# Optimization experiments

Measured on AMD Instinct MI355X. Metric: run time of the kernel, lower is better.

The kernel has to match this reference:

```python
import jax, jax.numpy as jnp
import numpy as np

N = 50000
E = 400000
IN_CH = 256
HEADS = 4
OUT_CH = 64
HID = HEADS * OUT_CH  # 256
ALPHA = 0.2
LN_EPS = 1e-5


def setup_inputs() -> dict:
    key = jax.random.key(0)
    ks = jax.random.split(key, 8)
    h = jax.random.normal(ks[0], (N, IN_CH), dtype=jnp.float32)
    edge_row = jax.random.randint(ks[1], (E,), 0, N, dtype=jnp.int32)
    edge_col = jax.random.randint(ks[2], (E,), 0, N, dtype=jnp.int32)
    # xavier-uniform-ish params
    def xavier(k, shape, fan_in, fan_out):
        lim = np.sqrt(6.0 / (fan_in + fan_out)).astype(np.float32)
        return jax.random.uniform(k, shape, jnp.float32, -lim, lim)
    W = xavier(ks[3], (IN_CH, HID), IN_CH, HID)              # Linear no bias
    attn_fc = xavier(ks[4], (HEADS, 2 * OUT_CH), 2 * OUT_CH, 1)
    ln_gamma = jnp.ones((HID,), jnp.float32)
    ln_beta = jnp.zeros((HID,), jnp.float32)
    ffn_w = xavier(ks[5], (HID, HID), HID, HID)
    ffn_b = jnp.zeros((HID,), jnp.float32)
    return {"h": h, "edge_row": edge_row, "edge_col": edge_col,
            "W": W, "attn_fc": attn_fc, "ln_gamma": ln_gamma,
            "ln_beta": ln_beta, "ffn_w": ffn_w, "ffn_b": ffn_b}


def reference(h, edge_row, edge_col, W, attn_fc, ln_gamma, ln_beta, ffn_w, ffn_b):
    # Wh: [N, H, D]
    Wh = (h @ W).reshape(N, HEADS, OUT_CH)
    Wh_i = Wh[edge_row]   # [E, H, D]
    Wh_j = Wh[edge_col]   # [E, H, D]
    # e = leakyrelu(cat(Wh_i, Wh_j) . attn_fc) per head -> split contraction
    a_src = attn_fc[:, :OUT_CH]  # [H, D]
    a_dst = attn_fc[:, OUT_CH:]  # [H, D]
    e = jnp.einsum('ehd,hd->eh', Wh_i, a_src) + jnp.einsum('ehd,hd->eh', Wh_j, a_dst)
    e = jax.nn.leaky_relu(e, negative_slope=ALPHA)
    # global max-shift exp (matches torch.exp(e - e.max(dim=0)))
    e = jnp.exp(e - jnp.max(e, axis=0, keepdims=True))  # [E, H]
    e_sum = jax.ops.segment_sum(e, edge_row, num_segments=N)  # [N, H]
    alpha = e / (e_sum[edge_row] + 1e-15)  # [E, H]  (dropout = identity in eval)
    # scatter-add weighted messages
    h_new = jax.ops.segment_sum(Wh_j * alpha[..., None], edge_row, num_segments=N)
    h_new = h_new.reshape(N, HID) + Wh.reshape(N, HID)  # residual (shapes match)
    # LayerNorm
    mu = jnp.mean(h_new, axis=-1, keepdims=True)
    var = jnp.var(h_new, axis=-1, keepdims=True)
    h_new = (h_new - mu) * jax.lax.rsqrt(var + LN_EPS) * ln_gamma + ln_beta
    # FFN: Linear + ReLU (+ dropout identity)
    return jax.nn.relu(h_new @ ffn_w + ffn_b)
```

## Files before the change

kernel.cpp:

```cpp
#include <hip/hip_runtime.h>
#include <hip/hip_bf16.h>

#define N_NODES 50000
#define E_EDGES 400000
#define IN_CH   256
#define HEADS   4
#define OUT_CH  64
#define HID     256
#define ALPHA   0.2f
#define LN_EPS  1e-5f

using f32x16 = __attribute__((ext_vector_type(16))) float;
using bf16x8 = __attribute__((ext_vector_type(8))) short;
using u16x8  = __attribute__((ext_vector_type(8))) unsigned short;
using u16x4  = __attribute__((ext_vector_type(4))) unsigned short;

typedef __attribute__((address_space(3))) void* lds_vp;
typedef const __attribute__((address_space(1))) void* gbl_vp;

__device__ __forceinline__ unsigned short f2bf(float f) {
    __hip_bfloat16 b = __float2bfloat16(f);
    return *(unsigned short*)&b;
}
__device__ __forceinline__ float bf2f(unsigned short u) {
    __hip_bfloat16 b = *(__hip_bfloat16*)&u;
    return __bfloat162float(b);
}

__global__ __launch_bounds__(256) void prep_kernel(
    const float* __restrict__ W, const float* __restrict__ ffn_w,
    unsigned short* __restrict__ Wt, unsigned short* __restrict__ Ft)
{
    int i = blockIdx.x * 256 + threadIdx.x;
    if (i < 65536) {
        int n = i >> 8, k = i & 255;
        Wt[i] = f2bf(W[k * 256 + n]);
    } else {
        int j = i - 65536;
        int n = j >> 8, k = j & 255;
        Ft[j] = f2bf(ffn_w[k * 256 + n]);
    }
}

template<bool A_IS_F32, bool RELU_BIAS>
__global__ __launch_bounds__(512, 2) void gemm_bres(
    const void* __restrict__ Av, const unsigned short* __restrict__ Bt,
    const float* __restrict__ bias, void* __restrict__ Cv, int M)
{
    __shared__ unsigned short Bs[256 * 256];

    const int tid = threadIdx.x;
    const int lane = tid & 63, wid = tid >> 6;

    #pragma unroll
    for (int i = 0; i < 16; i++) {
        int d = i * 512 + tid;
        int n = d >> 5, cp = d & 31;
        int cs = cp ^ (n & 31);
        const unsigned short* g = Bt + (size_t)n * 256 + cs * 8;
        __builtin_amdgcn_global_load_lds((gbl_vp)g, (lds_vp)&Bs[(size_t)d * 8],
                                         16, 0, 0);
    }
    __syncthreads();

    const int strip = wid * 256 + blockIdx.x;
    const int r0 = strip * 32;
    if (r0 >= M) return;

    const int q5 = lane & 31, kg = lane >> 5;
    const int rowc = min(r0 + q5, M - 1);

    f32x16 acc[8] = {};

    const float* Af = (const float*)Av;
    const unsigned short* Ab = (const unsigned short*)Av;

    float4 ra0, ra1; u16x8 rab;
    if (A_IS_F32) {
        const float* p = Af + (size_t)rowc * 256 + kg * 8;
        ra0 = *(const float4*)p; ra1 = *(const float4*)(p + 4);
    } else {
        rab = *(const u16x8*)(Ab + (size_t)rowc * 256 + kg * 8);
    }

    #pragma unroll 2
    for (int t = 0; t < 16; t++) {
        float4 nb0, nb1; u16x8 nbb;
        if (t + 1 < 16) {
            if (A_IS_F32) {
                const float* p = Af + (size_t)rowc * 256 + (t + 1) * 16 + kg * 8;
                nb0 = *(const float4*)p; nb1 = *(const float4*)(p + 4);
            } else {
                nbb = *(const u16x8*)(Ab + (size_t)rowc * 256 + (t + 1) * 16 + kg * 8);
            }
        }
        bf16x8 af;
        if (A_IS_F32) {
            union { unsigned int u[4]; bf16x8 v; } cv;
            cv.u[0] = (unsigned)f2bf(ra0.x) | ((unsigned)f2bf(ra0.y) << 16);
            cv.u[1] = (unsigned)f2bf(ra0.z) | ((unsigned)f2bf(ra0.w) << 16);
            cv.u[2] = (unsigned)f2bf(ra1.x) | ((unsigned)f2bf(ra1.y) << 16);
            cv.u[3] = (unsigned)f2bf(ra1.z) | ((unsigned)f2bf(ra1.w) << 16);
            af = cv.v;
        } else {
            union { u16x8 u; bf16x8 v; } cv; cv.u = rab; af = cv.v;
        }
        #pragma unroll
        for (int n = 0; n < 8; n++) {
            const bf16x8 bf = *(const bf16x8*)((const char*)Bs +
                (size_t)(n * 32 + q5) * 512 + (((t * 2 + kg) ^ q5) * 16));
            acc[n] = __builtin_amdgcn_mfma_f32_32x32x16_bf16(af, bf, acc[n], 0, 0, 0);
        }
        ra0 = nb0; ra1 = nb1; rab = nbb;
    }

    #pragma unroll
    for (int n = 0; n < 8; n++) {
        int gc = n * 32 + q5;
        float bv = RELU_BIAS ? bias[gc] : 0.f;
        #pragma unroll
        for (int reg = 0; reg < 16; reg++) {
            int rl = (reg & 3) + 8 * (reg >> 2) + 4 * kg;
            int gr = r0 + rl;
            if (gr >= M) continue;
            float v = acc[n][reg];
            if (RELU_BIAS) {
                v += bv; v = v > 0.f ? v : 0.f;
                ((float*)Cv)[(size_t)gr * 256 + gc] = v;
            } else {
                ((unsigned short*)Cv)[(size_t)gr * 256 + gc] = f2bf(v);
            }
        }
    }
}

__global__ __launch_bounds__(256) void scores_kernel(
    const unsigned short* __restrict__ Wh, const float* __restrict__ attn_fc,
    float* __restrict__ s_src, float* __restrict__ s_dst)
{
    const int lane = threadIdx.x & 63, wid = threadIdx.x >> 6;
    const int n = blockIdx.x * 4 + wid;
    const int h = lane >> 4;
    const int d0 = 4 * (lane & 15);
    u16x4 w = *(const u16x4*)(Wh + (size_t)n * HID + 4 * lane);
    float ps = 0.f, pd = 0.f;
    #pragma unroll
    for (int q = 0; q < 4; q++) {
        float wf = bf2f(w[q]);
        ps += wf * attn_fc[h * 128 + d0 + q];
        pd += wf * attn_fc[h * 128 + 64 + d0 + q];
    }
    #pragma unroll
    for (int off = 8; off; off >>= 1) {
        ps += __shfl_xor(ps, off, 16);
        pd += __shfl_xor(pd, off, 16);
    }
    if ((lane & 15) == 0) {
        s_src[n * HEADS + h] = ps;
        s_dst[n * HEADS + h] = pd;
    }
}

__global__ void hist_kernel(const int* __restrict__ erow, int* __restrict__ counts) {
    int e = blockIdx.x * blockDim.x + threadIdx.x;
    if (e < E_EDGES) atomicAdd(&counts[erow[e]], 1);
}

__global__ __launch_bounds__(256) void scanA_kernel(
    const int* __restrict__ counts, int* __restrict__ bsum)
{
    const int b = blockIdx.x, tid = threadIdx.x;
    int i0 = b * 512 + tid;
    int v = 0;
    if (i0 < N_NODES) v += counts[i0];
    if (i0 + 256 < N_NODES) v += counts[i0 + 256];
    #pragma unroll
    for (int off = 32; off; off >>= 1) v += __shfl_xor(v, off, 64);
    __shared__ int ws[4];
    if ((tid & 63) == 0) ws[tid >> 6] = v;
    __syncthreads();
    if (tid == 0) bsum[b] = ws[0] + ws[1] + ws[2] + ws[3];
}

__global__ __launch_bounds__(128) void scanB_kernel(
    const int* __restrict__ bsum, int* __restrict__ bscan, int nb)
{
    const int tid = threadIdx.x;
    const int lane = tid & 63, wid = tid >> 6;
    int val = (tid < nb) ? bsum[tid] : 0;
    int x = val;
    #pragma unroll
    for (int off = 1; off < 64; off <<= 1) {
        int y = __shfl_up(x, off, 64);
        if (lane >= off) x += y;
    }
    __shared__ int w0;
    if (tid == 63) w0 = x;
    __syncthreads();
    if (wid == 1) x += w0;
    if (tid < nb) bscan[tid] = x - val;
}

__global__ __launch_bounds__(512) void scanC_kernel(
    const int* __restrict__ counts, const int* __restrict__ bscan,
    int* __restrict__ offsets, int* __restrict__ cursor)
{
    const int b = blockIdx.x, tid = threadIdx.x;
    const int lane = tid & 63, wid = tid >> 6;
    const int i = b * 512 + tid;
    int v = (i < N_NODES) ? counts[i] : 0;
    int x = v;
    #pragma unroll
    for (int off = 1; off < 64; off <<= 1) {
        int y = __shfl_up(x, off, 64);
        if (lane >= off) x += y;
    }
    __shared__ int ws[8];
    if (lane == 63) ws[wid] = x;
    __syncthreads();
    if (wid == 0 && lane < 8) {
        int s = ws[lane];
        #pragma unroll
        for (int off = 1; off < 8; off <<= 1) {
            int y = __shfl_up(s, off, 8);
            if ((lane & 7) >= off) s += y;
        }
        ws[lane] = s;
    }
    __syncthreads();
    int prefix = (wid ? ws[wid - 1] : 0) + bscan[b];
    int excl = prefix + x - v;
    if (i < N_NODES) { offsets[i] = excl; cursor[i] = excl; }
    if (i == N_NODES - 1) offsets[N_NODES] = excl + v;
}

__global__ __launch_bounds__(256) void scatter_kernel(
    const int* __restrict__ erow, const int* __restrict__ ecol,
    const float* __restrict__ s_src, const float* __restrict__ s_dst,
    int* __restrict__ cursor, int* __restrict__ sorted_col,
    float4* __restrict__ sorted_w)
{
    int e = blockIdx.x * blockDim.x + threadIdx.x;
    if (e >= E_EDGES) return;
    int r = erow[e], c = ecol[e];
    float4 ss = ((const float4*)s_src)[r];
    float4 sd = ((const float4*)s_dst)[c];
    float sc[4] = {ss.x + sd.x, ss.y + sd.y, ss.z + sd.z, ss.w + sd.w};
    float4 w;
    float* wp = (float*)&w;
    #pragma unroll
    for (int h = 0; h < 4; h++) {
        float v = sc[h] > 0.f ? sc[h] : ALPHA * sc[h];
        wp[h] = __expf(v);
    }
    int pos = atomicAdd(&cursor[r], 1);
    sorted_col[pos] = c;
    sorted_w[pos] = w;
}

__global__ __launch_bounds__(256) void aggregate_ln_kernel(
    const unsigned short* __restrict__ Wh, const float* __restrict__ sorted_w,
    const int* __restrict__ offsets, const int* __restrict__ sorted_col,
    const float* __restrict__ ln_gamma, const float* __restrict__ ln_beta,
    unsigned short* __restrict__ h_ln)
{
    const int lane = threadIdx.x & 63, wid = threadIdx.x >> 6;
    const int n = blockIdx.x * 4 + wid;
    const int p = lane >> 5;
    const int q5 = lane & 31;
    const int c0 = q5 * 8;
    const int h = q5 >> 3;
    const int beg = offsets[n], end = offsets[n + 1];

    float acc[8] = {};
    float wsum = 0.f;
    for (int base = beg; base < end; base += 64) {
        int cnt = min(64, end - base);
        int cv = (base + lane < end) ? sorted_col[base + lane] : 0;
        int jj = 0;
        #pragma unroll 2
        for (; jj + 2 <= cnt; jj += 2) {
            int c = __shfl(cv, jj + p, 64);
            float w = sorted_w[(size_t)(base + jj + p) * 4 + h];
            u16x8 r = *(const u16x8*)(Wh + (size_t)c * HID + c0);
            wsum += w;
            #pragma unroll
            for (int k = 0; k < 8; k++) acc[k] += w * bf2f(r[k]);
        }
        if (jj < cnt) {
            int c = __shfl(cv, jj, 64);
            if (p == 0) {
                float w = sorted_w[(size_t)(base + jj) * 4 + h];
                u16x8 r = *(const u16x8*)(Wh + (size_t)c * HID + c0);
                wsum += w;
                #pragma unroll
                for (int k = 0; k < 8; k++) acc[k] += w * bf2f(r[k]);
            }
        }
    }
    wsum += __shfl_xor(wsum, 32, 64);
    #pragma unroll
    for (int k = 0; k < 8; k++) acc[k] += __shfl_xor(acc[k], 32, 64);

    u16x8 rr = *(const u16x8*)(Wh + (size_t)n * HID + c0);
    float inv_w = 1.f / (wsum + 1e-15f);
    float val[8];
    float s = 0.f;
    #pragma unroll
    for (int k = 0; k < 8; k++) {
        val[k] = acc[k] * inv_w + bf2f(rr[k]);
        s += val[k];
    }
    #pragma unroll
    for (int off = 16; off; off >>= 1) s += __shfl_xor(s, off, 64);
    float mu = s * (1.f / HID);
    float s2 = 0.f;
    #pragma unroll
    for (int k = 0; k < 8; k++) { float d = val[k] - mu; s2 += d * d; }
    #pragma unroll
    for (int off = 16; off; off >>= 1) s2 += __shfl_xor(s2, off, 64);
    float inv_std = rsqrtf(s2 * (1.f / HID) + LN_EPS);

    if (p == 0) {
        float4 g0 = *(const float4*)(ln_gamma + c0);
        float4 g1 = *(const float4*)(ln_gamma + c0 + 4);
        float4 b0 = *(const float4*)(ln_beta + c0);
        float4 b1 = *(const float4*)(ln_beta + c0 + 4);
        u16x8 outv;
        outv[0] = f2bf((val[0] - mu) * inv_std * g0.x + b0.x);
        outv[1] = f2bf((val[1] - mu) * inv_std * g0.y + b0.y);
        outv[2] = f2bf((val[2] - mu) * inv_std * g0.z + b0.z);
        outv[3] = f2bf((val[3] - mu) * inv_std * g0.w + b0.w);
        outv[4] = f2bf((val[4] - mu) * inv_std * g1.x + b1.x);
        outv[5] = f2bf((val[5] - mu) * inv_std * g1.y + b1.y);
        outv[6] = f2bf((val[6] - mu) * inv_std * g1.z + b1.z);
        outv[7] = f2bf((val[7] - mu) * inv_std * g1.w + b1.w);
        *(u16x8*)(h_ln + (size_t)n * HID + c0) = outv;
    }
}

extern "C" void kernel_launch(void* const* d_in, const int* in_sizes, int n_in,
                              void* d_out, int out_size, void* d_ws, size_t ws_size,
                              hipStream_t stream)
{
    const float* h        = (const float*)d_in[0];
    const int*   erow     = (const int*)  d_in[1];
    const int*   ecol     = (const int*)  d_in[2];
    const float* W        = (const float*)d_in[3];
    const float* attn_fc  = (const float*)d_in[4];
    const float* ln_gamma = (const float*)d_in[5];
    const float* ln_beta  = (const float*)d_in[6];
    const float* ffn_w    = (const float*)d_in[7];
    const float* ffn_b    = (const float*)d_in[8];
    float* out = (float*)d_out;

    unsigned short* Wh   = (unsigned short*)d_ws;
    unsigned short* h_ln = Wh + (size_t)N_NODES * HID;
    unsigned short* Wt   = h_ln + (size_t)N_NODES * HID;
    unsigned short* Ft   = Wt + 65536;
    float* s_src  = (float*)(Ft + 65536);
    float* s_dst  = s_src + N_NODES * HEADS;
    float* sorted_w = s_dst + N_NODES * HEADS;
    int*   counts = (int*)(sorted_w + (size_t)E_EDGES * HEADS);
    int*   offsets = counts + N_NODES;
    int*   cursor  = offsets + N_NODES + 1;
    int*   sorted_col = cursor + N_NODES;
    int*   bsum   = sorted_col + E_EDGES;
    int*   bscan  = bsum + 128;

    const int NB = (N_NODES + 511) / 512;

    hipMemsetAsync(counts, 0, N_NODES * sizeof(int), stream);
    prep_kernel<<<512, 256, 0, stream>>>(W, ffn_w, Wt, Ft);

    gemm_bres<true, false><<<256, 512, 0, stream>>>(h, Wt, nullptr, Wh, N_NODES);

    scores_kernel<<<N_NODES / 4, 256, 0, stream>>>(Wh, attn_fc, s_src, s_dst);
    hist_kernel<<<(E_EDGES + 255) / 256, 256, 0, stream>>>(erow, counts);
    scanA_kernel<<<NB, 256, 0, stream>>>(counts, bsum);
    scanB_kernel<<<1, 128, 0, stream>>>(bsum, bscan, NB);
    scanC_kernel<<<NB, 512, 0, stream>>>(counts, bscan, offsets, cursor);
    scatter_kernel<<<(E_EDGES + 255) / 256, 256, 0, stream>>>(
        erow, ecol, s_src, s_dst, cursor, sorted_col, (float4*)sorted_w);
    aggregate_ln_kernel<<<N_NODES / 4, 256, 0, stream>>>(
        Wh, sorted_w, offsets, sorted_col, ln_gamma, ln_beta, h_ln);

    gemm_bres<false, true><<<256, 512, 0, stream>>>(h_ln, Ft, ffn_b, out, N_NODES);
}
```

Before: 249.3 us.

## Fuse attention scores into first GEMM epilogue and deepen A-prefetch

Computes the per-node source/destination attention scores directly from the fp32 GEMM accumulators in the first GEMM's epilogue, removing the separate scores kernel and its re-read of Wh. The A-operand prefetch becomes a 4-deep register ring with the k-loop fully unrolled, to hide global load latency better. The aggregate loop unroll goes from 2 to 4. Scores are now computed from unrounded fp32 values instead of bf16 Wh, and the deeper prefetch plus score epilogue raise register pressure.

```diff
diff --git a/kernel.cpp b/kernel.cpp
--- a/kernel.cpp
+++ b/kernel.cpp
@@ -42,10 +42,12 @@
     }
 }
 
-template<bool A_IS_F32, bool RELU_BIAS>
+template<bool A_IS_F32, bool RELU_BIAS, bool SCORES>
 __global__ __launch_bounds__(512, 2) void gemm_bres(
     const void* __restrict__ Av, const unsigned short* __restrict__ Bt,
-    const float* __restrict__ bias, void* __restrict__ Cv, int M)
+    const float* __restrict__ bias, const float* __restrict__ attn_fc,
+    void* __restrict__ Cv, float* __restrict__ s_src, float* __restrict__ s_dst,
+    int M)
 {
     __shared__ unsigned short Bs[256 * 256];
 
@@ -75,43 +77,38 @@
     const float* Af = (const float*)Av;
     const unsigned short* Ab = (const unsigned short*)Av;
 
-    float4 ra0, ra1; u16x8 rab;
-    if (A_IS_F32) {
-        const float* p = Af + (size_t)rowc * 256 + kg * 8;
-        ra0 = *(const float4*)p; ra1 = *(const float4*)(p + 4);
-    } else {
-        rab = *(const u16x8*)(Ab + (size_t)rowc * 256 + kg * 8);
-    }
-
-    #pragma unroll 2
+    float4 pa[4], pb[4]; u16x8 pc[4];
+    auto loadA = [&](int t, int slot) {
+        if (A_IS_F32) {
+            const float* p = Af + (size_t)rowc * 256 + t * 16 + kg * 8;
+            pa[slot] = *(const float4*)p; pb[slot] = *(const float4*)(p + 4);
+        } else {
+            pc[slot] = *(const u16x8*)(Ab + (size_t)rowc * 256 + t * 16 + kg * 8);
+        }
+    };
+    loadA(0, 0); loadA(1, 1); loadA(2, 2); loadA(3, 3);
+
+    #pragma unroll
     for (int t = 0; t < 16; t++) {
-        float4 nb0, nb1; u16x8 nbb;
-        if (t + 1 < 16) {
-            if (A_IS_F32) {
-                const float* p = Af + (size_t)rowc * 256 + (t + 1) * 16 + kg * 8;
-                nb0 = *(const float4*)p; nb1 = *(const float4*)(p + 4);
-            } else {
-                nbb = *(const u16x8*)(Ab + (size_t)rowc * 256 + (t + 1) * 16 + kg * 8);
-            }
-        }
+        const int slot = t & 3;
         bf16x8 af;
         if (A_IS_F32) {
             union { unsigned int u[4]; bf16x8 v; } cv;
-            cv.u[0] = (unsigned)f2bf(ra0.x) | ((unsigned)f2bf(ra0.y) << 16);
-            cv.u[1] = (unsigned)f2bf(ra0.z) | ((unsigned)f2bf(ra0.w) << 16);
-            cv.u[2] = (unsigned)f2bf(ra1.x) | ((unsigned)f2bf(ra1.y) << 16);
-            cv.u[3] = (unsigned)f2bf(ra1.z) | ((unsigned)f2bf(ra1.w) << 16);
+            cv.u[0] = (unsigned)f2bf(pa[slot].x) | ((unsigned)f2bf(pa[slot].y) << 16);
+            cv.u[1] = (unsigned)f2bf(pa[slot].z) | ((unsigned)f2bf(pa[slot].w) << 16);
+            cv.u[2] = (unsigned)f2bf(pb[slot].x) | ((unsigned)f2bf(pb[slot].y) << 16);
+            cv.u[3] = (unsigned)f2bf(pb[slot].z) | ((unsigned)f2bf(pb[slot].w) << 16);
             af = cv.v;
         } else {
-            union { u16x8 u; bf16x8 v; } cv; cv.u = rab; af = cv.v;
-        }
+            union { u16x8 u; bf16x8 v; } cv; cv.u = pc[slot]; af = cv.v;
+        }
+        if (t + 4 < 16) loadA(t + 4, slot);
         #pragma unroll
         for (int n = 0; n < 8; n++) {
             const bf16x8 bf = *(const bf16x8*)((const char*)Bs +
                 (size_t)(n * 32 + q5) * 512 + (((t * 2 + kg) ^ q5) * 16));
             acc[n] = __builtin_amdgcn_mfma_f32_32x32x16_bf16(af, bf, acc[n], 0, 0, 0);
         }
-        ra0 = nb0; ra1 = nb1; rab = nbb;
     }
 
     #pragma unroll
@@ -132,32 +129,37 @@
             }
         }
     }
-}
-
-__global__ __launch_bounds__(256) void scores_kernel(
-    const unsigned short* __restrict__ Wh, const float* __restrict__ attn_fc,
-    float* __restrict__ s_src, float* __restrict__ s_dst)
-{
-    const int lane = threadIdx.x & 63, wid = threadIdx.x >> 6;
-    const int n = blockIdx.x * 4 + wid;
-    const int h = lane >> 4;
-    const int d0 = 4 * (lane & 15);
-    u16x4 w = *(const u16x4*)(Wh + (size_t)n * HID + 4 * lane);
-    float ps = 0.f, pd = 0.f;
-    #pragma unroll
-    for (int q = 0; q < 4; q++) {
-        float wf = bf2f(w[q]);
-        ps += wf * attn_fc[h * 128 + d0 + q];
-        pd += wf * attn_fc[h * 128 + 64 + d0 + q];
-    }
-    #pragma unroll
-    for (int off = 8; off; off >>= 1) {
-        ps += __shfl_xor(ps, off, 16);
-        pd += __shfl_xor(pd, off, 16);
-    }
-    if ((lane & 15) == 0) {
-        s_src[n * HEADS + h] = ps;
-        s_dst[n * HEADS + h] = pd;
+
+    if (SCORES) {
+        float as_[8], ad_[8];
+        #pragma unroll
+        for (int n = 0; n < 8; n++) {
+            int head = n >> 1, d = (n & 1) * 32 + q5;
+            as_[n] = attn_fc[head * 128 + d];
+            ad_[n] = attn_fc[head * 128 + 64 + d];
+        }
+        #pragma unroll
+        for (int reg = 0; reg < 16; reg++) {
+            int gr = r0 + (reg & 3) + 8 * (reg >> 2) + 4 * kg;
+            float ps[4] = {}, pd[4] = {};
+            #pragma unroll
+            for (int n = 0; n < 8; n++) {
+                ps[n >> 1] += acc[n][reg] * as_[n];
+                pd[n >> 1] += acc[n][reg] * ad_[n];
+            }
+            #pragma unroll
+            for (int off = 16; off; off >>= 1) {
+                #pragma unroll
+                for (int hh = 0; hh < 4; hh++) {
+                    ps[hh] += __shfl_xor(ps[hh], off, 32);
+                    pd[hh] += __shfl_xor(pd[hh], off, 32);
+                }
+            }
+            if (q5 == 0 && gr < M) {
+                *(float4*)(s_src + (size_t)gr * 4) = make_float4(ps[0], ps[1], ps[2], ps[3]);
+                *(float4*)(s_dst + (size_t)gr * 4) = make_float4(pd[0], pd[1], pd[2], pd[3]);
+            }
+        }
     }
 }
 
@@ -278,7 +280,7 @@
         int cnt = min(64, end - base);
         int cv = (base + lane < end) ? sorted_col[base + lane] : 0;
         int jj = 0;
-        #pragma unroll 2
+        #pragma unroll 4
         for (; jj + 2 <= cnt; jj += 2) {
             int c = __shfl(cv, jj + p, 64);
             float w = sorted_w[(size_t)(base + jj + p) * 4 + h];
@@ -373,9 +375,9 @@
     hipMemsetAsync(counts, 0, N_NODES * sizeof(int), stream);
     prep_kernel<<<512, 256, 0, stream>>>(W, ffn_w, Wt, Ft);
 
-    gemm_bres<true, false><<<256, 512, 0, stream>>>(h, Wt, nullptr, Wh, N_NODES);
-
-    scores_kernel<<<N_NODES / 4, 256, 0, stream>>>(Wh, attn_fc, s_src, s_dst);
+    gemm_bres<true, false, true><<<256, 512, 0, stream>>>(
+        h, Wt, nullptr, attn_fc, Wh, s_src, s_dst, N_NODES);
+
     hist_kernel<<<(E_EDGES + 255) / 256, 256, 0, stream>>>(erow, counts);
     scanA_kernel<<<NB, 256, 0, stream>>>(counts, bsum);
     scanB_kernel<<<1, 128, 0, stream>>>(bsum, bscan, NB);
@@ -385,5 +387,6 @@
     aggregate_ln_kernel<<<N_NODES / 4, 256, 0, stream>>>(
         Wh, sorted_w, offsets, sorted_col, ln_gamma, ln_beta, h_ln);
 
-    gemm_bres<false, true><<<256, 512, 0, stream>>>(h_ln, Ft, ffn_b, out, N_NODES);
-}
+    gemm_bres<false, true, false><<<256, 512, 0, stream>>>(
+        h_ln, Ft, ffn_b, nullptr, out, nullptr, nullptr, N_NODES);
+}
```

Result: no change. 252.5 us (+1.3%).

## Fuse aggregation+LayerNorm with FFN GEMM and deepen A-prefetch in GEMM

Applied to the files above, without the earlier changes.

Merges the aggregation/LayerNorm kernel with the FFN GEMM, so each 512-thread block aggregates 32 nodes into LDS and then runs the 32x256 MFMA FFN tile directly. This removes the bf16 h_ln round trip through global memory and one kernel launch. In exchange, every block reloads the full 128KB FFN weight matrix into LDS, which limits occupancy to one block per CU and costs about 1563 redundant weight loads. Separately, the first GEMM's A-operand prefetch goes from 1-deep to 4-deep with a fully unrolled loop, which raises register pressure.

```diff
diff --git a/kernel.cpp b/kernel.cpp
--- a/kernel.cpp
+++ b/kernel.cpp
@@ -75,43 +75,38 @@
     const float* Af = (const float*)Av;
     const unsigned short* Ab = (const unsigned short*)Av;
 
-    float4 ra0, ra1; u16x8 rab;
-    if (A_IS_F32) {
-        const float* p = Af + (size_t)rowc * 256 + kg * 8;
-        ra0 = *(const float4*)p; ra1 = *(const float4*)(p + 4);
-    } else {
-        rab = *(const u16x8*)(Ab + (size_t)rowc * 256 + kg * 8);
-    }
-
-    #pragma unroll 2
+    float4 pa[4], pb[4]; u16x8 pc[4];
+    auto loadA = [&](int t, int slot) {
+        if (A_IS_F32) {
+            const float* p = Af + (size_t)rowc * 256 + t * 16 + kg * 8;
+            pa[slot] = *(const float4*)p; pb[slot] = *(const float4*)(p + 4);
+        } else {
+            pc[slot] = *(const u16x8*)(Ab + (size_t)rowc * 256 + t * 16 + kg * 8);
+        }
+    };
+    loadA(0, 0); loadA(1, 1); loadA(2, 2); loadA(3, 3);
+
+    #pragma unroll
     for (int t = 0; t < 16; t++) {
-        float4 nb0, nb1; u16x8 nbb;
-        if (t + 1 < 16) {
-            if (A_IS_F32) {
-                const float* p = Af + (size_t)rowc * 256 + (t + 1) * 16 + kg * 8;
-                nb0 = *(const float4*)p; nb1 = *(const float4*)(p + 4);
-            } else {
-                nbb = *(const u16x8*)(Ab + (size_t)rowc * 256 + (t + 1) * 16 + kg * 8);
-            }
-        }
+        const int slot = t & 3;
         bf16x8 af;
         if (A_IS_F32) {
             union { unsigned int u[4]; bf16x8 v; } cv;
-            cv.u[0] = (unsigned)f2bf(ra0.x) | ((unsigned)f2bf(ra0.y) << 16);
-            cv.u[1] = (unsigned)f2bf(ra0.z) | ((unsigned)f2bf(ra0.w) << 16);
-            cv.u[2] = (unsigned)f2bf(ra1.x) | ((unsigned)f2bf(ra1.y) << 16);
-            cv.u[3] = (unsigned)f2bf(ra1.z) | ((unsigned)f2bf(ra1.w) << 16);
+            cv.u[0] = (unsigned)f2bf(pa[slot].x) | ((unsigned)f2bf(pa[slot].y) << 16);
+            cv.u[1] = (unsigned)f2bf(pa[slot].z) | ((unsigned)f2bf(pa[slot].w) << 16);
+            cv.u[2] = (unsigned)f2bf(pb[slot].x) | ((unsigned)f2bf(pb[slot].y) << 16);
+            cv.u[3] = (unsigned)f2bf(pb[slot].z) | ((unsigned)f2bf(pb[slot].w) << 16);
             af = cv.v;
         } else {
-            union { u16x8 u; bf16x8 v; } cv; cv.u = rab; af = cv.v;
-        }
+            union { u16x8 u; bf16x8 v; } cv; cv.u = pc[slot]; af = cv.v;
+        }
+        if (t + 4 < 16) loadA(t + 4, slot);
         #pragma unroll
         for (int n = 0; n < 8; n++) {
             const bf16x8 bf = *(const bf16x8*)((const char*)Bs +
                 (size_t)(n * 32 + q5) * 512 + (((t * 2 + kg) ^ q5) * 16));
             acc[n] = __builtin_amdgcn_mfma_f32_32x32x16_bf16(af, bf, acc[n], 0, 0, 0);
         }
-        ra0 = nb0; ra1 = nb1; rab = nbb;
     }
 
     #pragma unroll
@@ -258,84 +253,121 @@
     sorted_w[pos] = w;
 }
 
-__global__ __launch_bounds__(256) void aggregate_ln_kernel(
+__global__ __launch_bounds__(512) void agg_ffn_kernel(
     const unsigned short* __restrict__ Wh, const float* __restrict__ sorted_w,
     const int* __restrict__ offsets, const int* __restrict__ sorted_col,
     const float* __restrict__ ln_gamma, const float* __restrict__ ln_beta,
-    unsigned short* __restrict__ h_ln)
-{
-    const int lane = threadIdx.x & 63, wid = threadIdx.x >> 6;
-    const int n = blockIdx.x * 4 + wid;
+    const unsigned short* __restrict__ Ft, const float* __restrict__ ffn_b,
+    float* __restrict__ out)
+{
+    __shared__ unsigned short FtS[256 * 256];
+    __shared__ unsigned short Hs[32 * 256];
+
+    const int tid = threadIdx.x;
+    const int lane = tid & 63, wid = tid >> 6;
+
+    #pragma unroll
+    for (int i = 0; i < 16; i++) {
+        int d = i * 512 + tid;
+        int n = d >> 5, cp = d & 31;
+        int cs = cp ^ (n & 31);
+        const unsigned short* g = Ft + (size_t)n * 256 + cs * 8;
+        __builtin_amdgcn_global_load_lds((gbl_vp)g, (lds_vp)&FtS[(size_t)d * 8],
+                                         16, 0, 0);
+    }
+
+    const int n0 = blockIdx.x * 32;
     const int p = lane >> 5;
     const int q5 = lane & 31;
     const int c0 = q5 * 8;
     const int h = q5 >> 3;
-    const int beg = offsets[n], end = offsets[n + 1];
-
-    float acc[8] = {};
-    float wsum = 0.f;
-    for (int base = beg; base < end; base += 64) {
-        int cnt = min(64, end - base);
-        int cv = (base + lane < end) ? sorted_col[base + lane] : 0;
-        int jj = 0;
-        #pragma unroll 2
-        for (; jj + 2 <= cnt; jj += 2) {
-            int c = __shfl(cv, jj + p, 64);
-            float w = sorted_w[(size_t)(base + jj + p) * 4 + h];
-            u16x8 r = *(const u16x8*)(Wh + (size_t)c * HID + c0);
-            wsum += w;
-            #pragma unroll
-            for (int k = 0; k < 8; k++) acc[k] += w * bf2f(r[k]);
-        }
-        if (jj < cnt) {
-            int c = __shfl(cv, jj, 64);
-            if (p == 0) {
-                float w = sorted_w[(size_t)(base + jj) * 4 + h];
+
+    for (int nd = 0; nd < 4; nd++) {
+        const int lrow = wid * 4 + nd;
+        const int n = n0 + lrow;
+        if (n >= N_NODES) continue;
+        const int beg = offsets[n], end = offsets[n + 1];
+
+        float acc[8] = {};
+        float wsum = 0.f;
+        for (int base = beg; base < end; base += 64) {
+            int cnt = min(64, end - base);
+            int cv = (base + lane < end) ? sorted_col[base + lane] : 0;
+            int jj = 0;
+            #pragma unroll 2
+            for (; jj + 2 <= cnt; jj += 2) {
+                int c = __shfl(cv, jj + p, 64);
+                float w = sorted_w[(size_t)(base + jj + p) * 4 + h];
                 u16x8 r = *(const u16x8*)(Wh + (size_t)c * HID + c0);
                 wsum += w;
                 #pragma unroll
                 for (int k = 0; k < 8; k++) acc[k] += w * bf2f(r[k]);
             }
-        }
-    }
-    wsum += __shfl_xor(wsum, 32, 64);
-    #pragma unroll
-    for (int k = 0; k < 8; k++) acc[k] += __shfl_xor(acc[k], 32, 64);
-
-    u16x8 rr = *(const u16x8*)(Wh + (size_t)n * HID + c0);
-    float inv_w = 1.f / (wsum + 1e-15f);
-    float val[8];
-    float s = 0.f;
-    #pragma unroll
-    for (int k = 0; k < 8; k++) {
-        val[k] = acc[k] * inv_w + bf2f(rr[k]);
-        s += val[k];
-    }
-    #pragma unroll
-    for (int off = 16; off; off >>= 1) s += __shfl_xor(s, off, 64);
-    float mu = s * (1.f / HID);
-    float s2 = 0.f;
-    #pragma unroll
-    for (int k = 0; k < 8; k++) { float d = val[k] - mu; s2 += d * d; }
-    #pragma unroll
-    for (int off = 16; off; off >>= 1) s2 += __shfl_xor(s2, off, 64);
-    float inv_std = rsqrtf(s2 * (1.f / HID) + LN_EPS);
-
-    if (p == 0) {
-        float4 g0 = *(const float4*)(ln_gamma + c0);
-        float4 g1 = *(const float4*)(ln_gamma + c0 + 4);
-        float4 b0 = *(const float4*)(ln_beta + c0);
-        float4 b1 = *(const float4*)(ln_beta + c0 + 4);
-        u16x8 outv;
-        outv[0] = f2bf((val[0] - mu) * inv_std * g0.x + b0.x);
-        outv[1] = f2bf((val[1] - mu) * inv_std * g0.y + b0.y);
-        outv[2] = f2bf((val[2] - mu) * inv_std * g0.z + b0.z);
-        outv[3] = f2bf((val[3] - mu) * inv_std * g0.w + b0.w);
-        outv[4] = f2bf((val[4] - mu) * inv_std * g1.x + b1.x);
-        outv[5] = f2bf((val[5] - mu) * inv_std * g1.y + b1.y);
-        outv[6] = f2bf((val[6] - mu) * inv_std * g1.z + b1.z);
-        outv[7] = f2bf((val[7] - mu) * inv_std * g1.w + b1.w);
-        *(u16x8*)(h_ln + (size_t)n * HID + c0) = outv;
+            if (jj < cnt) {
+                int c = __shfl(cv, jj, 64);
+                if (p == 0) {
+                    float w = sorted_w[(size_t)(base + jj) * 4 + h];
+                    u16x8 r = *(const u16x8*)(Wh + (size_t)c * HID + c0);
+                    wsum += w;
+                    #pragma unroll
+                    for (int k = 0; k < 8; k++) acc[k] += w * bf2f(r[k]);
+                }
+            }
+        }
+        wsum += __shfl_xor(wsum, 32, 64);
+        #pragma unroll
+        for (int k = 0; k < 8; k++) acc[k] += __shfl_xor(acc[k], 32, 64);
+
+        u16x8 rr = *(const u16x8*)(Wh + (size_t)n * HID + c0);
+        float inv_w = 1.f / (wsum + 1e-15f);
+        float val[8];
+        float s = 0.f;
+        #pragma unroll
+        for (int k = 0; k < 8; k++) {
+            val[k] = acc[k] * inv_w + bf2f(rr[k]);
+            s += val[k];
+        }
+        #pragma unroll
+        for (int off = 16; off; off >>= 1) s += __shfl_xor(s, off, 64);
+        float mu = s * (1.f / HID);
+        float s2 = 0.f;
+        #pragma unroll
+        for (int k = 0; k < 8; k++) { float d = val[k] - mu; s2 += d * d; }
+        #pragma unroll
+        for (int off = 16; off; off >>= 1) s2 += __shfl_xor(s2, off, 64);
+        float inv_std = rsqrtf(s2 * (1.f / HID) + LN_EPS);
+
+        if (p == 0) {
+            u16x8 o;
+            #pragma unroll
+            for (int k = 0; k < 8; k++)
+                o[k] = f2bf((val[k] - mu) * inv_std * ln_gamma[c0 + k] + ln_beta[c0 + k]);
+            *(u16x8*)((char*)Hs + lrow * 512 + ((q5 ^ lrow) * 16)) = o;
+        }
+    }
+
+    __syncthreads();
+
+    const int kg = lane >> 5;
+    f32x16 acc2 = {};
+    #pragma unroll
+    for (int t = 0; t < 16; t++) {
+        const bf16x8 afr = *(const bf16x8*)((const char*)Hs +
+            q5 * 512 + (((t * 2 + kg) ^ q5) * 16));
+        const bf16x8 bfr = *(const bf16x8*)((const char*)FtS +
+            (size_t)(wid * 32 + q5) * 512 + (((t * 2 + kg) ^ q5) * 16));
+        acc2 = __builtin_amdgcn_mfma_f32_32x32x16_bf16(afr, bfr, acc2, 0, 0, 0);
+    }
+    const int gc = wid * 32 + q5;
+    const float bv = ffn_b[gc];
+    #pragma unroll
+    for (int reg = 0; reg < 16; reg++) {
+        int rl = (reg & 3) + 8 * (reg >> 2) + 4 * kg;
+        int gr = n0 + rl;
+        if (gr >= N_NODES) continue;
+        float v = acc2[reg] + bv;
+        v = v > 0.f ? v : 0.f;
+        out[(size_t)gr * 256 + gc] = v;
     }
 }
 
@@ -355,8 +387,7 @@
     float* out = (float*)d_out;
 
     unsigned short* Wh   = (unsigned short*)d_ws;
-    unsigned short* h_ln = Wh + (size_t)N_NODES * HID;
-    unsigned short* Wt   = h_ln + (size_t)N_NODES * HID;
+    unsigned short* Wt   = Wh + (size_t)N_NODES * HID;
     unsigned short* Ft   = Wt + 65536;
     float* s_src  = (float*)(Ft + 65536);
     float* s_dst  = s_src + N_NODES * HEADS;
@@ -369,6 +400,7 @@
     int*   bscan  = bsum + 128;
 
     const int NB = (N_NODES + 511) / 512;
+    const int GRID_AGG = (N_NODES + 31) / 32;
 
     hipMemsetAsync(counts, 0, N_NODES * sizeof(int), stream);
     prep_kernel<<<512, 256, 0, stream>>>(W, ffn_w, Wt, Ft);
@@ -382,8 +414,7 @@
     scanC_kernel<<<NB, 512, 0, stream>>>(counts, bscan, offsets, cursor);
     scatter_kernel<<<(E_EDGES + 255) / 256, 256, 0, stream>>>(
         erow, ecol, s_src, s_dst, cursor, sorted_col, (float4*)sorted_w);
-    aggregate_ln_kernel<<<N_NODES / 4, 256, 0, stream>>>(
-        Wh, sorted_w, offsets, sorted_col, ln_gamma, ln_beta, h_ln);
-
-    gemm_bres<false, true><<<256, 512, 0, stream>>>(h_ln, Ft, ffn_b, out, N_NODES);
-}
+
+    agg_ffn_kernel<<<GRID_AGG, 512, 0, stream>>>(
+        Wh, sorted_w, offsets, sorted_col, ln_gamma, ln_beta, Ft, ffn_b, out);
+}
```

Result: slower. 309.6 us (+24.2%).

## Split GEMM output columns across two blocks and double-buffer A loads

Applied to the files above, without the earlier changes.

Each GEMM block now computes only half of the 256 output columns, so the B tile held in LDS shrinks to 64KB. The grid doubles to 512 blocks and the launch bound allows 4 blocks per CU, which raises occupancy and spreads work across more CUs. The A-row prefetch becomes a two-deep register buffer loaded two k-steps ahead. The cost is that each A row is read twice, once per column half, and every block still loads its own B half.

```diff
diff --git a/kernel.cpp b/kernel.cpp
--- a/kernel.cpp
+++ b/kernel.cpp
@@ -43,80 +43,78 @@
 }
 
 template<bool A_IS_F32, bool RELU_BIAS>
-__global__ __launch_bounds__(512, 2) void gemm_bres(
+__global__ __launch_bounds__(512, 4) void gemm_bres(
     const void* __restrict__ Av, const unsigned short* __restrict__ Bt,
     const float* __restrict__ bias, void* __restrict__ Cv, int M)
 {
-    __shared__ unsigned short Bs[256 * 256];
+    __shared__ unsigned short Bs[128 * 256];
 
     const int tid = threadIdx.x;
     const int lane = tid & 63, wid = tid >> 6;
-
-    #pragma unroll
-    for (int i = 0; i < 16; i++) {
+    const int colhalf = blockIdx.x & 1;
+    const int col0 = colhalf * 128;
+    const int sb = blockIdx.x >> 1;
+
+    #pragma unroll
+    for (int i = 0; i < 8; i++) {
         int d = i * 512 + tid;
         int n = d >> 5, cp = d & 31;
         int cs = cp ^ (n & 31);
-        const unsigned short* g = Bt + (size_t)n * 256 + cs * 8;
+        const unsigned short* g = Bt + (size_t)(col0 + n) * 256 + cs * 8;
         __builtin_amdgcn_global_load_lds((gbl_vp)g, (lds_vp)&Bs[(size_t)d * 8],
                                          16, 0, 0);
     }
     __syncthreads();
 
-    const int strip = wid * 256 + blockIdx.x;
+    const int strip = wid * 256 + sb;
     const int r0 = strip * 32;
     if (r0 >= M) return;
 
     const int q5 = lane & 31, kg = lane >> 5;
     const int rowc = min(r0 + q5, M - 1);
 
-    f32x16 acc[8] = {};
+    f32x16 acc[4] = {};
 
     const float* Af = (const float*)Av;
     const unsigned short* Ab = (const unsigned short*)Av;
 
-    float4 ra0, ra1; u16x8 rab;
-    if (A_IS_F32) {
-        const float* p = Af + (size_t)rowc * 256 + kg * 8;
-        ra0 = *(const float4*)p; ra1 = *(const float4*)(p + 4);
-    } else {
-        rab = *(const u16x8*)(Ab + (size_t)rowc * 256 + kg * 8);
-    }
-
-    #pragma unroll 2
+    float4 pa[2], pb[2]; u16x8 pc[2];
+    auto loadA = [&](int t, int slot) {
+        if (A_IS_F32) {
+            const float* p = Af + (size_t)rowc * 256 + t * 16 + kg * 8;
+            pa[slot] = *(const float4*)p; pb[slot] = *(const float4*)(p + 4);
+        } else {
+            pc[slot] = *(const u16x8*)(Ab + (size_t)rowc * 256 + t * 16 + kg * 8);
+        }
+    };
+    loadA(0, 0); loadA(1, 1);
+
+    #pragma unroll
     for (int t = 0; t < 16; t++) {
-        float4 nb0, nb1; u16x8 nbb;
-        if (t + 1 < 16) {
-            if (A_IS_F32) {
-                const float* p = Af + (size_t)rowc * 256 + (t + 1) * 16 + kg * 8;
-                nb0 = *(const float4*)p; nb1 = *(const float4*)(p + 4);
-            } else {
-                nbb = *(const u16x8*)(Ab + (size_t)rowc * 256 + (t + 1) * 16 + kg * 8);
-            }
-        }
+        const int slot = t & 1;
         bf16x8 af;
         if (A_IS_F32) {
             union { unsigned int u[4]; bf16x8 v; } cv;
-            cv.u[0] = (unsigned)f2bf(ra0.x) | ((unsigned)f2bf(ra0.y) << 16);
-            cv.u[1] = (unsigned)f2bf(ra0.z) | ((unsigned)f2bf(ra0.w) << 16);
-            cv.u[2] = (unsigned)f2bf(ra1.x) | ((unsigned)f2bf(ra1.y) << 16);
-            cv.u[3] = (unsigned)f2bf(ra1.z) | ((unsigned)f2bf(ra1.w) << 16);
+            cv.u[0] = (unsigned)f2bf(pa[slot].x) | ((unsigned)f2bf(pa[slot].y) << 16);
+            cv.u[1] = (unsigned)f2bf(pa[slot].z) | ((unsigned)f2bf(pa[slot].w) << 16);
+            cv.u[2] = (unsigned)f2bf(pb[slot].x) | ((unsigned)f2bf(pb[slot].y) << 16);
+            cv.u[3] = (unsigned)f2bf(pb[slot].z) | ((unsigned)f2bf(pb[slot].w) << 16);
             af = cv.v;
         } else {
-            union { u16x8 u; bf16x8 v; } cv; cv.u = rab; af = cv.v;
-        }
+            union { u16x8 u; bf16x8 v; } cv; cv.u = pc[slot]; af = cv.v;
+        }
+        if (t + 2 < 16) loadA(t + 2, slot);
         #pragma unroll
-        for (int n = 0; n < 8; n++) {
+        for (int n = 0; n < 4; n++) {
             const bf16x8 bf = *(const bf16x8*)((const char*)Bs +
                 (size_t)(n * 32 + q5) * 512 + (((t * 2 + kg) ^ q5) * 16));
             acc[n] = __builtin_amdgcn_mfma_f32_32x32x16_bf16(af, bf, acc[n], 0, 0, 0);
         }
-        ra0 = nb0; ra1 = nb1; rab = nbb;
-    }
-
-    #pragma unroll
-    for (int n = 0; n < 8; n++) {
-        int gc = n * 32 + q5;
+    }
+
+    #pragma unroll
+    for (int n = 0; n < 4; n++) {
+        int gc = col0 + n * 32 + q5;
         float bv = RELU_BIAS ? bias[gc] : 0.f;
         #pragma unroll
         for (int reg = 0; reg < 16; reg++) {
@@ -373,7 +371,7 @@
     hipMemsetAsync(counts, 0, N_NODES * sizeof(int), stream);
     prep_kernel<<<512, 256, 0, stream>>>(W, ffn_w, Wt, Ft);
 
-    gemm_bres<true, false><<<256, 512, 0, stream>>>(h, Wt, nullptr, Wh, N_NODES);
+    gemm_bres<true, false><<<512, 512, 0, stream>>>(h, Wt, nullptr, Wh, N_NODES);
 
     scores_kernel<<<N_NODES / 4, 256, 0, stream>>>(Wh, attn_fc, s_src, s_dst);
     hist_kernel<<<(E_EDGES + 255) / 256, 256, 0, stream>>>(erow, counts);
@@ -385,5 +383,5 @@
     aggregate_ln_kernel<<<N_NODES / 4, 256, 0, stream>>>(
         Wh, sorted_w, offsets, sorted_col, ln_gamma, ln_beta, h_ln);
 
-    gemm_bres<false, true><<<256, 512, 0, stream>>>(h_ln, Ft, ffn_b, out, N_NODES);
-}
+    gemm_bres<false, true><<<512, 512, 0, stream>>>(h_ln, Ft, ffn_b, out, N_NODES);
+}
```

Measured after the change: 249.8 us. No clear change (+0.2%).
